# Kernel tuning notes

Measured on AMD Instinct MI355X. Metric: run time of the kernel, lower is better.

The kernel has to match this reference:

```python
import jax, jax.numpy as jnp
import numpy as np
from jax import lax

EPS = 1e-8

def _norm(v, eps=EPS):
    # matches torch F.normalize: v / max(||v||, eps)
    return v / jnp.maximum(jnp.linalg.norm(v, axis=-1, keepdims=True), eps)

def keep_r6(r6):
    v1 = _norm(r6[..., :3])
    v2 = r6[..., 3:6]
    v2 = v2 - jnp.sum(v2 * v1, axis=-1, keepdims=True) * v1
    v2n = jnp.linalg.norm(v2, axis=-1, keepdims=True)
    mask = (v2n < 1e-6).astype(r6.dtype)
    e1 = jnp.array([1.0, 0.0, 0.0], dtype=r6.dtype)
    e2 = jnp.array([0.0, 1.0, 0.0], dtype=r6.dtype)
    dot = jnp.abs(jnp.sum(v1 * e1, axis=-1, keepdims=True))
    fb = jnp.where(dot < 0.9, e1, e2)
    fb_v2 = jnp.cross(v1, jnp.broadcast_to(fb, v1.shape), axis=-1)
    v2 = (1.0 - mask) * v2 + mask * fb_v2
    v2 = _norm(v2)
    return jnp.concatenate([v1, v2], axis=-1)

def r6_to_matrix(r6):
    r6 = keep_r6(r6)
    v1, v2 = r6[..., :3], r6[..., 3:6]
    v3 = jnp.cross(v1, v2, axis=-1)
    R = jnp.stack([v1, v2, v3], axis=-1)  # columns v1,v2,v3
    det = jnp.linalg.det(R)
    return R * jnp.sign(det)[..., None, None]

def instance_norm(x, eps=1e-5):
    # InstanceNorm3d, affine=False: per-(B,C) stats over spatial dims, biased var
    mu = jnp.mean(x, axis=(2, 3, 4), keepdims=True)
    var = jnp.mean((x - mu) ** 2, axis=(2, 3, 4), keepdims=True)
    return (x - mu) * lax.rsqrt(var + eps)

def conv1x1(x, w, b):
    return jnp.einsum('oc,bcdhw->bodhw', w[:, :, 0, 0, 0], x) + b[None, :, None, None, None]

def conv3_circ(x, w, b):
    xp = jnp.pad(x, ((0, 0), (0, 0), (1, 1), (1, 1), (1, 1)), mode='wrap')
    out = lax.conv_general_dilated(xp, w, (1, 1, 1), 'VALID',
                                   dimension_numbers=('NCDHW', 'OIDHW', 'NCDHW'))
    return out + b[None, :, None, None, None]

def _gelu(t):
    return jax.nn.gelu(t, approximate=False)

def _forward(x, pos_emb, qkv_w, qkv_b, lp1_w, lp1_b, lp2_w, lp2_b,
             mod1_w, mod1_b, mod2_w, mod2_b, pa_w, pa_b,
             R6_d, R6_h, R6_w, proj_w, proj_b):
    B, C, D, H, W = x.shape
    NH = pa_w.shape[0]
    HD = C // NH
    NV = HD // 3
    scale = HD ** (-0.5)

    # PositionalProcessing (deterministic; computed once, reused for all 3 axes)
    local = conv1x1(_gelu(instance_norm(conv3_circ(pos_emb, lp1_w, lp1_b))), lp2_w, lp2_b)
    mod = jax.nn.sigmoid(conv1x1(_gelu(instance_norm(conv1x1(local, mod1_w, mod1_b))), mod2_w, mod2_b))
    x_mod = x * mod
    pos_attn = _gelu(instance_norm(conv1x1(pos_emb, pa_w, pa_b)))  # [B,NH,D,H,W]

    axes = [
        (R6_d, (0, 3, 4, 1, 2), (0, 4, 3, 1, 2)),  # depth
        (R6_h, (0, 2, 4, 1, 3), (0, 4, 1, 3, 2)),  # height
        (R6_w, (0, 2, 3, 1, 4), (0, 4, 1, 2, 3)),  # width
    ]
    out_sum = 0.0
    for R6, perm, inv in axes:
        xp = jnp.transpose(x_mod, perm)      # [B, A1, A2, C, L]
        Bb, A1, A2, _, L = xp.shape
        bd = Bb * A1 * A2
        xl = jnp.swapaxes(xp.reshape(bd, C, L), -1, -2)  # [bd, L, C]
        qkv = (xl @ qkv_w.T + qkv_b).reshape(bd, L, 3, NH, HD)
        qkv = jnp.transpose(qkv, (2, 0, 3, 1, 4))
        q, k, v = qkv[0], qkv[1], qkv[2]     # [bd, NH, L, HD]
        R = r6_to_matrix(keep_r6(R6))[0]     # [NH, 3, 3]

        def rot(t):
            tv = t.reshape(bd, NH, L, NV, 3)
            return jnp.einsum('hij,bhlvj->bhlvi', R, tv).reshape(bd, NH, L, HD)

        attn = jnp.einsum('bhqd,bhkd->bhqk', rot(q), rot(k)) * scale
        pa = jnp.transpose(pos_attn, perm).reshape(bd, NH, L)
        attn = jax.nn.softmax(attn + pa[..., None], axis=-1)
        o = jnp.einsum('bhqk,bhkd->bhqd', attn, v)      # [bd, NH, L, HD]
        o = jnp.swapaxes(o, 1, 2).reshape(Bb, A1, A2, L, C)
        out_sum = out_sum + jnp.transpose(o, inv)        # [B, C, D, H, W]
    return conv1x1(out_sum, proj_w, proj_b)


def setup_inputs() -> dict:
    key = jax.random.key(0)
    ks = jax.random.split(key, 20)
    B, C, D, H, W, NH = 2, 96, 40, 40, 40, 4

    def rn(k, shape, s=0.05):
        return jax.random.normal(k, shape, dtype=jnp.float32) * s

    return {
        'x': jax.random.normal(ks[0], (B, C, D, H, W), dtype=jnp.float32),
        'pos_emb': jax.random.normal(ks[1], (B, C, D, H, W), dtype=jnp.float32),
        'qkv_w': rn(ks[2], (3 * C, C)), 'qkv_b': rn(ks[3], (3 * C,)),
        'lp1_w': rn(ks[4], (C, C, 3, 3, 3)), 'lp1_b': rn(ks[5], (C,)),
        'lp2_w': rn(ks[6], (C, C, 1, 1, 1)), 'lp2_b': rn(ks[7], (C,)),
        'mod1_w': rn(ks[8], (C, C, 1, 1, 1)), 'mod1_b': rn(ks[9], (C,)),
        'mod2_w': rn(ks[10], (C, C, 1, 1, 1)), 'mod2_b': rn(ks[11], (C,)),
        'pa_w': rn(ks[12], (NH, C, 1, 1, 1)), 'pa_b': rn(ks[13], (NH,)),
        'R6_d': jax.random.normal(ks[14], (1, NH, 6), dtype=jnp.float32),
        'R6_h': jax.random.normal(ks[15], (1, NH, 6), dtype=jnp.float32),
        'R6_w': jax.random.normal(ks[16], (1, NH, 6), dtype=jnp.float32),
        'proj_w': rn(ks[17], (C, C, 1, 1, 1)), 'proj_b': rn(ks[18], (C,)),
    }


def reference(x, pos_emb, qkv_w, qkv_b, lp1_w, lp1_b, lp2_w, lp2_b,
              mod1_w, mod1_b, mod2_w, mod2_b, pa_w, pa_b,
              R6_d, R6_h, R6_w, proj_w, proj_b):
    return _forward(x, pos_emb, qkv_w, qkv_b, lp1_w, lp1_b, lp2_w, lp2_b,
                    mod1_w, mod1_b, mod2_w, mod2_b, pa_w, pa_b,
                    R6_d, R6_h, R6_w, proj_w, proj_b)
```

## Files before the change

kernel.cpp:

```cpp
#include <hip/hip_runtime.h>


typedef __attribute__((ext_vector_type(8))) _Float16 half8;
typedef __attribute__((ext_vector_type(2))) _Float16 half2;
typedef __attribute__((ext_vector_type(16))) float floatx16;

static __device__ __forceinline__ half2 h2(unsigned int u) {
    return __builtin_bit_cast(half2, u);
}
static __device__ __forceinline__ float fdot2(unsigned int a, unsigned int b, float c) {
    return __builtin_amdgcn_fdot2(h2(a), h2(b), c, false);
}

__global__ void k_zero(float* __restrict__ p) {
    int t = threadIdx.x;
    for (int i = t; i < 768; i += 256) p[i] = 0.f;
}

__global__ __launch_bounds__(256) void k_cvt_in(const float* __restrict__ pos,
                                                _Float16* __restrict__ in_t) {
    __shared__ _Float16 lds[64][97];
    int bid = blockIdx.x;
    int xcd = bid & 7, idx = bid >> 3;
    int L = xcd * 125 + (idx >> 1);
    int b = L / 500;
    int s0 = (L % 500) * 128 + (idx & 1) * 64;
    int t = threadIdx.x;
    for (int i = t; i < 6144; i += 256) {
        int c = i / 64, sl = i % 64;
        lds[sl][c] = (_Float16)pos[(b * 96 + c) * 64000 + s0 + sl];
    }
    __syncthreads();
    _Float16* outp = in_t + ((size_t)b * 64000 + s0) * 96;
    for (int i = t; i < 6144; i += 256) {
        int sl = i / 96, c = i % 96;
        outp[i] = lds[sl][c];
    }
}

__global__ void k_cvt_w(const float* __restrict__ w, _Float16* __restrict__ wf) {
    int i = blockIdx.x * 256 + threadIdx.x;
    if (i < 248832) {
        int e = i & 7;
        int r2 = i >> 3;
        int row = r2 & 31;
        int r3 = r2 >> 5;
        int kg = r3 & 1;
        int r4 = r3 >> 1;
        int j = r4 % 6;
        int r5 = r4 / 6;
        int mt = r5 % 3;
        int tap = r5 / 3;
        int m = mt * 32 + row, c = j * 16 + kg * 8 + e;
        wf[i] = (_Float16)w[(m * 96 + c) * 27 + tap];
    }
}

__global__ void k_cvt_f16(const float* __restrict__ w, _Float16* __restrict__ o, int n) {
    int i = blockIdx.x * 256 + threadIdx.x;
    if (i < n) o[i] = (_Float16)w[i];
}

__global__ __launch_bounds__(256) void k_fold(const float* __restrict__ lp2_w,
                                              const float* __restrict__ lp2_b,
                                              const float* __restrict__ mod1_w,
                                              const float* __restrict__ mod1_b,
                                              _Float16* __restrict__ wfold,
                                              float* __restrict__ bfold) {
    int i = blockIdx.x * 256 + threadIdx.x;
    if (i < 9216) {
        int o = i / 96, c = i % 96;
        float a = 0.f;
        for (int k = 0; k < 96; k++) a += mod1_w[o * 96 + k] * lp2_w[k * 96 + c];
        wfold[i] = (_Float16)a;
    }
    if (blockIdx.x == 0 && threadIdx.x < 96) {
        int o = threadIdx.x;
        float a = mod1_b[o];
        for (int k = 0; k < 96; k++) a += mod1_w[o * 96 + k] * lp2_b[k];
        bfold[o] = a;
    }
}

__global__ __launch_bounds__(128) void k_conv3_v4(const _Float16* __restrict__ in_t,
                                                  const _Float16* __restrict__ wfp,
                                                  const float* __restrict__ bias,
                                                  _Float16* __restrict__ c3,
                                                  float* __restrict__ raw0) {
    __shared__ _Float16 st[128 * 98];
    __shared__ float bsh[96];
    int* tbl = (int*)st;
    int t = threadIdx.x;
    int bid = blockIdx.x;
    { int xcd = bid & 7; bid = xcd * 125 + (bid >> 3); }
    int b = bid / 500, s0 = (bid % 500) * 128;

    for (int u = t; u < 27 * 128; u += 128) {
        int tap = u >> 7, nl = u & 127;
        int kd = tap / 9, kh = (tap / 3) % 3, kw = tap % 3;
        int s = s0 + nl;
        int d = s / 1600, r = s - d * 1600;
        int h = r / 40, w = r - h * 40;
        int ds = d + kd - 1; if (ds < 0) ds += 40; else if (ds >= 40) ds -= 40;
        int hs = h + kh - 1; if (hs < 0) hs += 40; else if (hs >= 40) hs -= 40;
        int wv2 = w + kw - 1; if (wv2 < 0) wv2 += 40; else if (wv2 >= 40) wv2 -= 40;
        tbl[u] = ((ds * 1600 + hs * 40 + wv2) * 96) * 2;
    }
    if (t < 96) bsh[t] = bias[t];
    __syncthreads();

    int wv = t >> 6, lane = t & 63;
    int n31 = lane & 31, kg = lane >> 5;
    const char* inb = (const char*)(in_t + (size_t)b * 64000 * 96) + kg * 16;
    const _Float16* wl = wfp + lane * 8;

    floatx16 acc[3][2];
#pragma unroll
    for (int mt = 0; mt < 3; mt++)
#pragma unroll
        for (int nt = 0; nt < 2; nt++)
#pragma unroll
            for (int r = 0; r < 16; r++) acc[mt][nt][r] = 0.f;

    for (int tap = 0; tap < 27; tap++) {
        int ta0 = tbl[tap * 128 + wv * 64 + n31];
        int ta1 = tbl[tap * 128 + wv * 64 + 32 + n31];
        const char* pb0 = inb + ta0;
        const char* pb1 = inb + ta1;
        const _Float16* wt = wl + tap * 9216;
#pragma unroll
        for (int j = 0; j < 6; j++) {
            half8 b0 = *(const half8*)(pb0 + j * 32);
            half8 b1 = *(const half8*)(pb1 + j * 32);
            half8 a0 = *(const half8*)(wt + (0 * 6 + j) * 512);
            half8 a1 = *(const half8*)(wt + (1 * 6 + j) * 512);
            half8 a2 = *(const half8*)(wt + (2 * 6 + j) * 512);
            acc[0][0] = __builtin_amdgcn_mfma_f32_32x32x16_f16(a0, b0, acc[0][0], 0, 0, 0);
            acc[0][1] = __builtin_amdgcn_mfma_f32_32x32x16_f16(a0, b1, acc[0][1], 0, 0, 0);
            acc[1][0] = __builtin_amdgcn_mfma_f32_32x32x16_f16(a1, b0, acc[1][0], 0, 0, 0);
            acc[1][1] = __builtin_amdgcn_mfma_f32_32x32x16_f16(a1, b1, acc[1][1], 0, 0, 0);
            acc[2][0] = __builtin_amdgcn_mfma_f32_32x32x16_f16(a2, b0, acc[2][0], 0, 0, 0);
            acc[2][1] = __builtin_amdgcn_mfma_f32_32x32x16_f16(a2, b1, acc[2][1], 0, 0, 0);
        }
    }

    __syncthreads();
#pragma unroll
    for (int mt = 0; mt < 3; mt++)
#pragma unroll
        for (int nt = 0; nt < 2; nt++)
#pragma unroll
            for (int r = 0; r < 16; r++) {
                int m = mt * 32 + (r & 3) + 8 * (r >> 2) + 4 * kg;
                int sl = wv * 64 + nt * 32 + n31;
                st[sl * 98 + m] = (_Float16)(acc[mt][nt][r] + bsh[m]);
            }
    __syncthreads();

    unsigned int* dst = (unsigned int*)(c3 + ((size_t)(b * 64000 + s0)) * 96);
    for (int i = t; i < 6144; i += 128) {
        int row = i / 48, sg = i % 48;
        __builtin_nontemporal_store(*(const unsigned int*)&st[row * 98 + sg * 2], &dst[i]);
    }
    if (t < 96) {
        float S = 0.f, Q = 0.f;
        for (int r2 = 0; r2 < 128; r2++) {
            float f = (float)st[r2 * 98 + t];
            S += f; Q += f * f;
        }
        atomicAdd(&raw0[(b * 96 + t) * 2], S);
        atomicAdd(&raw0[(b * 96 + t) * 2 + 1], Q);
    }
}

__global__ void k_finalize(const float* __restrict__ raw, float2* __restrict__ sf) {
    int t = threadIdx.x;
    if (t < 192) {
        float S = raw[t * 2], Q = raw[t * 2 + 1];
        float mu = S * (1.f / 64000.f);
        float var = Q * (1.f / 64000.f) - mu * mu;
        sf[t] = make_float2(mu, rsqrtf(var + 1e-5f));
    }
}

template <int MODE>
__global__ __launch_bounds__(256) void k_gemm96(const _Float16* __restrict__ in,
                                                const _Float16* __restrict__ w,
                                                const float* __restrict__ bias,
                                                const float2* __restrict__ sf,
                                                const float* __restrict__ xg,
                                                float* __restrict__ rawout,
                                                _Float16* __restrict__ outp) {
    __shared__ _Float16 un[12544];
    __shared__ float bias_s[96];
    __shared__ float2 sfs[96];
    int t = threadIdx.x, bid = blockIdx.x;
    int b = bid / 500, s0 = (bid % 500) * 128;
    for (int i = t; i < 1152; i += 256) ((uint4*)un)[i] = ((const uint4*)w)[i];
    if (t < 96) { bias_s[t] = bias[t]; sfs[t] = sf[b * 96 + t]; }
    __syncthreads();

    int ws = t >> 6, lane = t & 63;
    int n = lane & 31, kg = lane >> 5;
    int p = ws * 32 + n;
    const uint4* brow = (const uint4*)(in + ((size_t)(b * 64000 + s0 + p)) * 96);
    uint4 bf[6];
#pragma unroll
    for (int kc = 0; kc < 6; kc++) bf[kc] = brow[kc * 2 + kg];

#pragma unroll
    for (int kc = 0; kc < 6; kc++) {
        half8 hv = __builtin_bit_cast(half8, bf[kc]);
        _Float16 o[8];
#pragma unroll
        for (int e = 0; e < 8; e++) {
            float2 s2 = sfs[kc * 16 + kg * 8 + e];
            float u = ((float)hv[e] - s2.x) * s2.y;
            o[e] = (_Float16)(0.5f * u * (1.f + erff(u * 0.70710678118654752f)));
        }
        bf[kc] = *(const uint4*)o;
    }

    floatx16 acc[3];
#pragma unroll
    for (int mt = 0; mt < 3; mt++)
#pragma unroll
        for (int r = 0; r < 16; r++) acc[mt][r] = 0.f;
#pragma unroll
    for (int kc = 0; kc < 6; kc++) {
        half8 bfh = __builtin_bit_cast(half8, bf[kc]);
#pragma unroll
        for (int mt = 0; mt < 3; mt++) {
            uint4 au = *(const uint4*)&un[(mt * 32 + n) * 96 + kc * 16 + kg * 8];
            acc[mt] = __builtin_amdgcn_mfma_f32_32x32x16_f16(__builtin_bit_cast(half8, au), bfh, acc[mt], 0, 0, 0);
        }
    }
    __syncthreads();

#pragma unroll
    for (int mt = 0; mt < 3; mt++)
#pragma unroll
        for (int r = 0; r < 16; r++) {
            int m = mt * 32 + (r & 3) + 8 * (r >> 2) + 4 * kg;
            int sl = ws * 32 + n;
            float v = acc[mt][r] + bias_s[m];
            if (MODE == 1) {
                v = 1.f / (1.f + __expf(-v));
                v *= xg[((size_t)(b * 96 + m)) * 64000 + s0 + sl];
            }
            un[sl * 98 + m] = (_Float16)v;
        }
    __syncthreads();

    if (MODE == 0 && t < 96) {
        float S = 0.f, Q = 0.f;
        for (int r2 = 0; r2 < 128; r2++) {
            float f = (float)un[r2 * 98 + t];
            S += f; Q += f * f;
        }
        atomicAdd(&rawout[(b * 96 + t) * 2], S);
        atomicAdd(&rawout[(b * 96 + t) * 2 + 1], Q);
    }

    unsigned int* dst = (unsigned int*)(outp + ((size_t)(b * 64000 + s0)) * 96);
    for (int i = t; i < 6144; i += 256) {
        int row = i / 48, sg = i % 48;
        dst[i] = *(const unsigned int*)&un[row * 98 + sg * 2];
    }
}

__global__ __launch_bounds__(256) void k_qkv(const _Float16* __restrict__ xt,
                                             const _Float16* __restrict__ wq,
                                             const float* __restrict__ qb,
                                             _Float16* __restrict__ qA) {
    __shared__ _Float16 smem[27648];
    __shared__ float bias_s[288];
    int t = threadIdx.x;
    int bid = blockIdx.x;
    int b = bid / 500;
    int s0 = (bid % 500) * 128;

    for (int i = t; i < 3456; i += 256) ((uint4*)smem)[i] = ((const uint4*)wq)[i];
    for (int i = t; i < 288; i += 256) bias_s[i] = qb[i];
    __syncthreads();

    int ws = t >> 6, lane = t & 63;
    int n = lane & 31, kg = lane >> 5;
    int p = ws * 32 + n;

    const uint4* brow = (const uint4*)(xt + ((size_t)(b * 64000 + s0 + p)) * 96);
    uint4 bf[6];
#pragma unroll
    for (int kc = 0; kc < 6; kc++) bf[kc] = brow[kc * 2 + kg];

    floatx16 acc[9];
#pragma unroll
    for (int mt = 0; mt < 9; mt++)
#pragma unroll
        for (int r = 0; r < 16; r++) acc[mt][r] = 0.f;

#pragma unroll
    for (int kc = 0; kc < 6; kc++) {
        half8 bfh = __builtin_bit_cast(half8, bf[kc]);
#pragma unroll
        for (int mt = 0; mt < 9; mt++) {
            uint4 au = *(const uint4*)&smem[(mt * 32 + n) * 96 + kc * 16 + kg * 8];
            acc[mt] = __builtin_amdgcn_mfma_f32_32x32x16_f16(__builtin_bit_cast(half8, au), bfh, acc[mt], 0, 0, 0);
        }
    }

    const float scale = 0.20412414523193154f;
    for (int q = 0; q < 2; q++) {
        __syncthreads();
        if ((ws >> 1) == q) {
            int pl = (ws & 1) * 32 + n;
#pragma unroll
            for (int mt = 0; mt < 9; mt++)
#pragma unroll
                for (int g = 0; g < 4; g++) {
                    int m0 = mt * 32 + g * 8 + kg * 4;
                    _Float16 tm[4];
#pragma unroll
                    for (int j = 0; j < 4; j++) {
                        float v = acc[mt][g * 4 + j] + bias_s[m0 + j];
                        if (m0 + j < 96) v *= scale;
                        tm[j] = (_Float16)v;
                    }
                    *(uint2*)&smem[pl * 296 + m0] = *(uint2*)tm;
                }
        }
        __syncthreads();
        for (int idx = t; idx < 2304; idx += 256) {
            int pl = idx / 36, seg = idx % 36;
            int s = s0 + q * 64 + pl;
            uint4 v = *(const uint4*)&smem[pl * 296 + seg * 8];
            *(uint4*)&qA[((size_t)(b * 64000 + s)) * 288 + seg * 8] = v;
        }
    }
}

template <int AXIS, bool ACC>
__global__ __launch_bounds__(320, 3) void k_attn(const _Float16* __restrict__ qA,
                                                 _Float16* __restrict__ osum) {
    __shared__ _Float16 kk[8352];
    __shared__ _Float16 vT[7744];
    int t = threadIdx.x;
    int bid = blockIdx.x;
    int b = bid / 800;
    int r0 = (bid % 800) * 2;

    auto smap = [&](int r, int l) -> int {
        if (AXIS == 0) return l * 1600 + r;
        else if (AXIS == 1) { int d = r / 40, w = r % 40; return d * 1600 + l * 40 + w; }
        else return r * 40 + l;
    };
    const uint4* src = (const uint4*)qA;
    for (int i = t; i < 960; i += 320) {
        int line = i / 480, key = (i % 480) / 12, seg = i % 12;
        int row = b * 64000 + smap(r0 + line, key);
        ((uint4*)kk)[i] = src[(size_t)row * 36 + 12 + seg];
    }
    for (int i = t; i < 960; i += 320) {
        int line = i / 480, key = (i % 480) / 12, seg = i % 12;
        int row = b * 64000 + smap(r0 + line, key);
        uint4 v = src[(size_t)row * 36 + 24 + seg];
        _Float16 tmp[8];
        *(uint4*)tmp = v;
#pragma unroll
        for (int e = 0; e < 8; e++) {
            int hdg = seg * 8 + e;
            vT[(line * 4 + hdg / 24) * 968 + (hdg % 24) * 40 + key] = tmp[e];
        }
    }

    int line = t / 160, head = (t % 160) / 40, ql = t % 40;
    int rr = r0 + line;
    unsigned int qu[12];
    {
        const uint4* qp = (const uint4*)(qA + ((size_t)(b * 64000 + smap(rr, ql))) * 288 + head * 24);
#pragma unroll
        for (int j = 0; j < 3; j++) *(uint4*)&qu[j * 4] = qp[j];
    }
    __syncthreads();

    float s[40];
    const uint4* kbase = (const uint4*)kk + line * 480 + head * 3;
#pragma unroll 4
    for (int key = 0; key < 40; key++) {
        unsigned int kku[12];
#pragma unroll
        for (int j = 0; j < 3; j++) *(uint4*)&kku[j * 4] = kbase[key * 12 + j];
        float a = 0.f;
#pragma unroll
        for (int i = 0; i < 12; i++) a = fdot2(kku[i], qu[i], a);
        s[key] = a;
    }

    float mx = -1e30f;
#pragma unroll
    for (int i = 0; i < 40; i++) mx = fmaxf(mx, s[i]);
    float sum = 0.f;
#pragma unroll
    for (int i = 0; i < 40; i++) { s[i] = __expf(s[i] - mx); sum += s[i]; }
    float inv = 1.f / sum;

    unsigned int pw[20];
#pragma unroll
    for (int i = 0; i < 20; i++) {
        half2 a = { (_Float16)(s[2 * i] * inv), (_Float16)(s[2 * i + 1] * inv) };
        pw[i] = __builtin_bit_cast(unsigned int, a);
    }

    __syncthreads();

    float o[24];
    const uint4* vbase = (const uint4*)vT + (line * 4 + head) * 121;
#pragma unroll 2
    for (int hd = 0; hd < 24; hd++) {
        unsigned int vv[20];
#pragma unroll
        for (int j = 0; j < 5; j++) *(uint4*)&vv[j * 4] = vbase[hd * 5 + j];
        float a = 0.f;
#pragma unroll
        for (int i = 0; i < 20; i++) a = fdot2(vv[i], pw[i], a);
        o[hd] = a;
    }

    {
        _Float16 tm[24];
#pragma unroll
        for (int j = 0; j < 24; j++) tm[j] = (_Float16)o[j];
        _Float16* dA = &kk[(line * 40 + ql) * 104 + head * 24];
#pragma unroll
        for (int j = 0; j < 3; j++) ((uint4*)dA)[j] = ((uint4*)tm)[j];
    }
    __syncthreads();

    uint4* dst = (uint4*)osum;
    for (int i = t; i < 960; i += 320) {
        int row = i / 12, seg = i % 12;
        int s2 = smap(r0 + row / 40, row % 40);
        size_t di = ((size_t)(b * 64000 + s2)) * 12 + seg;
        uint4 v = *(const uint4*)&kk[row * 104 + seg * 8];
        if (ACC) {
            half8 a = __builtin_bit_cast(half8, dst[di]);
            half8 c = __builtin_bit_cast(half8, v);
            dst[di] = __builtin_bit_cast(uint4, a + c);
        } else {
            dst[di] = v;
        }
    }
}

__global__ __launch_bounds__(256) void k_proj(const _Float16* __restrict__ osum,
                                              const _Float16* __restrict__ wp,
                                              const float* __restrict__ pb,
                                              float* __restrict__ out) {
    __shared__ _Float16 A[9216];
    __shared__ float bias_s[96];
    int t = threadIdx.x;
    int bid = blockIdx.x;
    int b = bid / 500;
    int s0 = (bid % 500) * 128;
    for (int i = t; i < 1152; i += 256) ((uint4*)A)[i] = ((const uint4*)wp)[i];
    if (t < 96) bias_s[t] = pb[t];
    __syncthreads();

    int ws = t >> 6, lane = t & 63;
    int n = lane & 31, kg = lane >> 5;
    int s = s0 + ws * 32 + n;

    const uint4* brow = (const uint4*)(osum + ((size_t)(b * 64000 + s0 + ws * 32 + n)) * 96);
    uint4 bf[6];
#pragma unroll
    for (int kc = 0; kc < 6; kc++) bf[kc] = brow[kc * 2 + kg];

    floatx16 acc[3];
#pragma unroll
    for (int mt = 0; mt < 3; mt++)
#pragma unroll
        for (int r = 0; r < 16; r++) acc[mt][r] = 0.f;

#pragma unroll
    for (int kc = 0; kc < 6; kc++) {
        half8 bfh = __builtin_bit_cast(half8, bf[kc]);
#pragma unroll
        for (int mt = 0; mt < 3; mt++) {
            uint4 au = *(const uint4*)&A[(mt * 32 + n) * 96 + kc * 16 + kg * 8];
            acc[mt] = __builtin_amdgcn_mfma_f32_32x32x16_f16(__builtin_bit_cast(half8, au), bfh, acc[mt], 0, 0, 0);
        }
    }

#pragma unroll
    for (int mt = 0; mt < 3; mt++)
#pragma unroll
        for (int r = 0; r < 16; r++) {
            int m = mt * 32 + (r & 3) + 8 * (r >> 2) + 4 * kg;
            out[((size_t)(b * 96 + m)) * 64000 + s] = acc[mt][r] + bias_s[m];
        }
}

extern "C" void kernel_launch(void* const* d_in, const int* in_sizes, int n_in,
                              void* d_out, int out_size, void* d_ws, size_t ws_size,
                              hipStream_t stream) {
    const float* x      = (const float*)d_in[0];
    const float* pos    = (const float*)d_in[1];
    const float* qkv_w  = (const float*)d_in[2];
    const float* qkv_b  = (const float*)d_in[3];
    const float* lp1_w  = (const float*)d_in[4];
    const float* lp1_b  = (const float*)d_in[5];
    const float* lp2_w  = (const float*)d_in[6];
    const float* lp2_b  = (const float*)d_in[7];
    const float* mod1_w = (const float*)d_in[8];
    const float* mod1_b = (const float*)d_in[9];
    const float* mod2_w = (const float*)d_in[10];
    const float* mod2_b = (const float*)d_in[11];
    const float* proj_w = (const float*)d_in[17];
    const float* proj_b = (const float*)d_in[18];
    float* out = (float*)d_out;
    float* ws = (float*)d_ws;

    _Float16* bufA = (_Float16*)ws;
    _Float16* bufB = (_Float16*)(ws + 6144000);
    _Float16* qA   = (_Float16*)(ws + 12288000);
    _Float16* in_t = qA;
    _Float16* wf   = (_Float16*)(ws + 30720000);
    _Float16* wq   = (_Float16*)(ws + 30844416);
    _Float16* wpj  = (_Float16*)(ws + 30858240);
    _Float16* wfold= (_Float16*)(ws + 30862848);
    _Float16* wm2  = (_Float16*)(ws + 30867456);
    float* bfold   = ws + 30872064;
    float* raw     = ws + 30872160;
    float2* sf0    = (float2*)(ws + 30872928);
    float2* sf1    = (float2*)(ws + 30873312);
    float* raw0 = raw, *raw1 = raw + 384;

    k_zero<<<1, 256, 0, stream>>>(raw);
    k_cvt_in<<<2000, 256, 0, stream>>>(pos, in_t);
    k_cvt_w<<<972, 256, 0, stream>>>(lp1_w, wf);
    k_fold<<<36, 256, 0, stream>>>(lp2_w, lp2_b, mod1_w, mod1_b, wfold, bfold);
    k_cvt_f16<<<36, 256, 0, stream>>>(mod2_w, wm2, 9216);
    k_cvt_f16<<<108, 256, 0, stream>>>(qkv_w, wq, 27648);
    k_cvt_f16<<<36, 256, 0, stream>>>(proj_w, wpj, 9216);

    k_conv3_v4<<<1000, 128, 0, stream>>>(in_t, wf, lp1_b, bufA, raw0);
    k_finalize<<<1, 256, 0, stream>>>(raw0, sf0);
    k_gemm96<0><<<1000, 256, 0, stream>>>(bufA, wfold, bfold, sf0, nullptr, raw1, bufB);
    k_finalize<<<1, 256, 0, stream>>>(raw1, sf1);
    k_gemm96<1><<<1000, 256, 0, stream>>>(bufB, wm2, mod2_b, sf1, x, nullptr, bufA);

    k_qkv<<<1000, 256, 0, stream>>>(bufA, wq, qkv_b, qA);
    k_attn<2, false><<<1600, 320, 0, stream>>>(qA, bufB);
    k_attn<0, true ><<<1600, 320, 0, stream>>>(qA, bufB);
    k_attn<1, true ><<<1600, 320, 0, stream>>>(qA, bufB);

    k_proj<<<1000, 256, 0, stream>>>(bufB, wpj, proj_b, out);
}
```

Before: 748.0 us.

## Stage conv3 input and weight tiles in LDS with larger 256-voxel blocks

The circular 3x3x3 conv kernel now handles 256 voxels per 256-thread block. For each tap it cooperatively copies the shifted input rows and that tap's weight slice into LDS, then feeds the MFMA operands from LDS instead of gathering straight from global memory per lane. Block-to-XCD remapping is updated to match the new conv block count, and added to the gemm96 and qkv kernels for L2 locality. The cost is two barriers per tap and about 80KB of LDS per block, which limits occupancy and leaves load and compute unoverlapped.

```diff
diff --git a/kernel.cpp b/kernel.cpp
--- a/kernel.cpp
+++ b/kernel.cpp
@@ -21,10 +21,13 @@
                                                 _Float16* __restrict__ in_t) {
     __shared__ _Float16 lds[64][97];
     int bid = blockIdx.x;
-    int xcd = bid & 7, idx = bid >> 3;
-    int L = xcd * 125 + (idx >> 1);
-    int b = L / 500;
-    int s0 = (L % 500) * 128 + (idx & 1) * 64;
+    int xcd = bid & 7, k = bid >> 3;
+    int L;
+    if (xcd < 4) L = xcd * 63 + (k >> 2);
+    else { if (k >= 248) return; L = 252 + (xcd - 4) * 62 + (k >> 2); }
+    int q = k & 3;
+    int b = L / 250;
+    int s0 = (L % 250) * 256 + q * 64;
     int t = threadIdx.x;
     for (int i = t; i < 6144; i += 256) {
         int c = i / 64, sl = i % 64;
@@ -82,37 +85,53 @@
     }
 }
 
-__global__ __launch_bounds__(128) void k_conv3_v4(const _Float16* __restrict__ in_t,
+__global__ __launch_bounds__(256) void k_conv3_v5(const _Float16* __restrict__ in_t,
                                                   const _Float16* __restrict__ wfp,
                                                   const float* __restrict__ bias,
                                                   _Float16* __restrict__ c3,
                                                   float* __restrict__ raw0) {
-    __shared__ _Float16 st[128 * 98];
-    __shared__ float bsh[96];
-    int* tbl = (int*)st;
+    __shared__ __align__(16) char smem[81280];
+    _Float16* stf = (_Float16*)smem;
+    int* adh = (int*)(smem + 71680);
+    float* bsh = (float*)(smem + 80896);
     int t = threadIdx.x;
     int bid = blockIdx.x;
-    { int xcd = bid & 7; bid = xcd * 125 + (bid >> 3); }
-    int b = bid / 500, s0 = (bid % 500) * 128;
-
-    for (int u = t; u < 27 * 128; u += 128) {
-        int tap = u >> 7, nl = u & 127;
-        int kd = tap / 9, kh = (tap / 3) % 3, kw = tap % 3;
-        int s = s0 + nl;
-        int d = s / 1600, r = s - d * 1600;
-        int h = r / 40, w = r - h * 40;
-        int ds = d + kd - 1; if (ds < 0) ds += 40; else if (ds >= 40) ds -= 40;
-        int hs = h + kh - 1; if (hs < 0) hs += 40; else if (hs >= 40) hs -= 40;
-        int wv2 = w + kw - 1; if (wv2 < 0) wv2 += 40; else if (wv2 >= 40) wv2 -= 40;
-        tbl[u] = ((ds * 1600 + hs * 40 + wv2) * 96) * 2;
+    { int xcd = bid & 7, idx = bid >> 3;
+      bid = (xcd < 4) ? (xcd * 63 + idx) : (252 + (xcd - 4) * 62 + idx); }
+    int b = bid / 250, s0 = (bid % 250) * 256;
+
+    {
+        int s = s0 + t;
+        int d = s / 1600, rr = s - d * 1600;
+        int h = rr / 40;
+#pragma unroll
+        for (int kd = 0; kd < 3; kd++) {
+            int dd = d + kd - 1; if (dd < 0) dd += 40; else if (dd >= 40) dd -= 40;
+#pragma unroll
+            for (int kh = 0; kh < 3; kh++) {
+                int hh = h + kh - 1; if (hh < 0) hh += 40; else if (hh >= 40) hh -= 40;
+                adh[(kd * 3 + kh) * 256 + t] = dd * 307200 + hh * 7680;
+            }
+        }
     }
     if (t < 96) bsh[t] = bias[t];
-    __syncthreads();
+
+    int r12[12], c16[12], w12[12];
+#pragma unroll
+    for (int k = 0; k < 12; k++) {
+        int idx = k * 256 + t;
+        int r = idx / 12;
+        r12[k] = r;
+        c16[k] = (idx - r * 12) * 16;
+        w12[k] = (s0 + r) % 40;
+    }
 
     int wv = t >> 6, lane = t & 63;
     int n31 = lane & 31, kg = lane >> 5;
-    const char* inb = (const char*)(in_t + (size_t)b * 64000 * 96) + kg * 16;
-    const _Float16* wl = wfp + lane * 8;
+    const char* inb = (const char*)(in_t + (size_t)b * 64000 * 96);
+    const _Float16* sA = (const _Float16*)(smem + 53248);
+    const char* bB0 = smem + (wv * 64 + n31) * 208 + kg * 16;
+    const char* bB1 = smem + (wv * 64 + 32 + n31) * 208 + kg * 16;
 
     floatx16 acc[3][2];
 #pragma unroll
@@ -122,29 +141,46 @@
 #pragma unroll
             for (int r = 0; r < 16; r++) acc[mt][nt][r] = 0.f;
 
-    for (int tap = 0; tap < 27; tap++) {
-        int ta0 = tbl[tap * 128 + wv * 64 + n31];
-        int ta1 = tbl[tap * 128 + wv * 64 + 32 + n31];
-        const char* pb0 = inb + ta0;
-        const char* pb1 = inb + ta1;
-        const _Float16* wt = wl + tap * 9216;
-#pragma unroll
-        for (int j = 0; j < 6; j++) {
-            half8 b0 = *(const half8*)(pb0 + j * 32);
-            half8 b1 = *(const half8*)(pb1 + j * 32);
-            half8 a0 = *(const half8*)(wt + (0 * 6 + j) * 512);
-            half8 a1 = *(const half8*)(wt + (1 * 6 + j) * 512);
-            half8 a2 = *(const half8*)(wt + (2 * 6 + j) * 512);
-            acc[0][0] = __builtin_amdgcn_mfma_f32_32x32x16_f16(a0, b0, acc[0][0], 0, 0, 0);
-            acc[0][1] = __builtin_amdgcn_mfma_f32_32x32x16_f16(a0, b1, acc[0][1], 0, 0, 0);
-            acc[1][0] = __builtin_amdgcn_mfma_f32_32x32x16_f16(a1, b0, acc[1][0], 0, 0, 0);
-            acc[1][1] = __builtin_amdgcn_mfma_f32_32x32x16_f16(a1, b1, acc[1][1], 0, 0, 0);
-            acc[2][0] = __builtin_amdgcn_mfma_f32_32x32x16_f16(a2, b0, acc[2][0], 0, 0, 0);
-            acc[2][1] = __builtin_amdgcn_mfma_f32_32x32x16_f16(a2, b1, acc[2][1], 0, 0, 0);
-        }
-    }
-
-    __syncthreads();
+    __syncthreads();
+
+    for (int kdh = 0; kdh < 9; kdh++) {
+        int ro[12];
+#pragma unroll
+        for (int k = 0; k < 12; k++) ro[k] = adh[kdh * 256 + r12[k]];
+        for (int kw = 0; kw < 3; kw++) {
+            int tap = kdh * 3 + kw;
+#pragma unroll
+            for (int k = 0; k < 12; k++) {
+                int ww = w12[k] + kw - 1; if (ww < 0) ww += 40; else if (ww >= 40) ww -= 40;
+                uint4 v = *(const uint4*)(inb + ro[k] + ww * 192 + c16[k]);
+                *(uint4*)(smem + r12[k] * 208 + c16[k]) = v;
+            }
+            {
+                const uint4* asrc = (const uint4*)(wfp + tap * 9216);
+                uint4* adst = (uint4*)(smem + 53248);
+#pragma unroll
+                for (int k = 0; k < 4; k++) adst[k * 256 + t] = asrc[k * 256 + t];
+                if (t < 128) adst[1024 + t] = asrc[1024 + t];
+            }
+            __syncthreads();
+#pragma unroll
+            for (int j = 0; j < 6; j++) {
+                half8 b0 = *(const half8*)(bB0 + j * 32);
+                half8 b1 = *(const half8*)(bB1 + j * 32);
+                half8 a0 = *(const half8*)(sA + ((0 * 6 + j) * 64 + lane) * 8);
+                half8 a1 = *(const half8*)(sA + ((1 * 6 + j) * 64 + lane) * 8);
+                half8 a2 = *(const half8*)(sA + ((2 * 6 + j) * 64 + lane) * 8);
+                acc[0][0] = __builtin_amdgcn_mfma_f32_32x32x16_f16(a0, b0, acc[0][0], 0, 0, 0);
+                acc[0][1] = __builtin_amdgcn_mfma_f32_32x32x16_f16(a0, b1, acc[0][1], 0, 0, 0);
+                acc[1][0] = __builtin_amdgcn_mfma_f32_32x32x16_f16(a1, b0, acc[1][0], 0, 0, 0);
+                acc[1][1] = __builtin_amdgcn_mfma_f32_32x32x16_f16(a1, b1, acc[1][1], 0, 0, 0);
+                acc[2][0] = __builtin_amdgcn_mfma_f32_32x32x16_f16(a2, b0, acc[2][0], 0, 0, 0);
+                acc[2][1] = __builtin_amdgcn_mfma_f32_32x32x16_f16(a2, b1, acc[2][1], 0, 0, 0);
+            }
+            __syncthreads();
+        }
+    }
+
 #pragma unroll
     for (int mt = 0; mt < 3; mt++)
 #pragma unroll
@@ -153,19 +189,19 @@
             for (int r = 0; r < 16; r++) {
                 int m = mt * 32 + (r & 3) + 8 * (r >> 2) + 4 * kg;
                 int sl = wv * 64 + nt * 32 + n31;
-                st[sl * 98 + m] = (_Float16)(acc[mt][nt][r] + bsh[m]);
+                stf[sl * 98 + m] = (_Float16)(acc[mt][nt][r] + bsh[m]);
             }
     __syncthreads();
 
     unsigned int* dst = (unsigned int*)(c3 + ((size_t)(b * 64000 + s0)) * 96);
-    for (int i = t; i < 6144; i += 128) {
+    for (int i = t; i < 12288; i += 256) {
         int row = i / 48, sg = i % 48;
-        __builtin_nontemporal_store(*(const unsigned int*)&st[row * 98 + sg * 2], &dst[i]);
+        __builtin_nontemporal_store(*(const unsigned int*)&stf[row * 98 + sg * 2], &dst[i]);
     }
     if (t < 96) {
         float S = 0.f, Q = 0.f;
-        for (int r2 = 0; r2 < 128; r2++) {
-            float f = (float)st[r2 * 98 + t];
+        for (int r2 = 0; r2 < 256; r2++) {
+            float f = (float)stf[r2 * 98 + t];
             S += f; Q += f * f;
         }
         atomicAdd(&raw0[(b * 96 + t) * 2], S);
@@ -195,6 +231,7 @@
     __shared__ float bias_s[96];
     __shared__ float2 sfs[96];
     int t = threadIdx.x, bid = blockIdx.x;
+    { int xcd = bid & 7; bid = xcd * 125 + (bid >> 3); }
     int b = bid / 500, s0 = (bid % 500) * 128;
     for (int i = t; i < 1152; i += 256) ((uint4*)un)[i] = ((const uint4*)w)[i];
     if (t < 96) { bias_s[t] = bias[t]; sfs[t] = sf[b * 96 + t]; }
@@ -277,6 +314,7 @@
     __shared__ float bias_s[288];
     int t = threadIdx.x;
     int bid = blockIdx.x;
+    { int xcd = bid & 7; bid = xcd * 125 + (bid >> 3); }
     int b = bid / 500;
     int s0 = (bid % 500) * 128;
 
@@ -536,14 +574,14 @@
     float* raw0 = raw, *raw1 = raw + 384;
 
     k_zero<<<1, 256, 0, stream>>>(raw);
-    k_cvt_in<<<2000, 256, 0, stream>>>(pos, in_t);
+    k_cvt_in<<<2016, 256, 0, stream>>>(pos, in_t);
     k_cvt_w<<<972, 256, 0, stream>>>(lp1_w, wf);
     k_fold<<<36, 256, 0, stream>>>(lp2_w, lp2_b, mod1_w, mod1_b, wfold, bfold);
     k_cvt_f16<<<36, 256, 0, stream>>>(mod2_w, wm2, 9216);
     k_cvt_f16<<<108, 256, 0, stream>>>(qkv_w, wq, 27648);
     k_cvt_f16<<<36, 256, 0, stream>>>(proj_w, wpj, 9216);
 
-    k_conv3_v4<<<1000, 128, 0, stream>>>(in_t, wf, lp1_b, bufA, raw0);
+    k_conv3_v5<<<500, 256, 0, stream>>>(in_t, wf, lp1_b, bufA, raw0);
     k_finalize<<<1, 256, 0, stream>>>(raw0, sf0);
     k_gemm96<0><<<1000, 256, 0, stream>>>(bufA, wfold, bfold, sf0, nullptr, raw1, bufB);
     k_finalize<<<1, 256, 0, stream>>>(raw1, sf1);
```

Measured after the change: 809.4 us. 8.2% more time.
